# Kernel optimization log

Measured on AMD Instinct MI355X. Metric: run time of the kernel, lower is better.

The kernel has to match this reference:

```python
import jax, jax.numpy as jnp
import numpy as np

SEQ_LEN = 4096
N_FEAT = 2048
N_PADD = 128


def setup_inputs() -> dict:
    key = jax.random.key(0)
    kx, kw = jax.random.split(key)
    x = jax.random.normal(kx, (SEQ_LEN, N_FEAT), dtype=jnp.float32)
    # Fused QKV dense: features = 3 * n_feat
    W = jax.random.normal(kw, (N_FEAT, 3 * N_FEAT), dtype=jnp.float32) * (1.0 / np.sqrt(N_FEAT))
    b = jnp.zeros((3 * N_FEAT,), dtype=jnp.float32)
    return {"x": x, "W": W, "b": b, "n_padd": N_PADD}


def reference(x, W, b, n_padd):
    # Fused QKV projection, split along feature axis (as in nn.Dense + jnp.split)
    qkv = x @ W + b  # [S, 3F]
    q, k, v = jnp.split(qkv, 3, axis=1)  # each [S, F]
    S, F = q.shape
    idx = jnp.arange(S)
    # scores[i, j] = q_i . k_j / sqrt(F)
    scores = (q @ k.T) * (1.0 / jnp.sqrt(jnp.float32(F)))  # [S, S]
    seq_mask = idx >= n_padd                      # valid (non-padding) positions
    causal = idx[None, :] <= idx[:, None]         # j <= i
    mask = causal & seq_mask[None, :]             # kernel: causal_mask & seq_mask
    row_valid = seq_mask                          # rows < n_padd are not computed/stored
    neg_inf = jnp.float32(-jnp.inf)
    scores = jnp.where(mask, scores, neg_inf)
    # Fully-masked (padding) rows would softmax to NaN; neutralize then zero output.
    scores = jnp.where(row_valid[:, None], scores, 0.0)
    att = jax.nn.softmax(scores, axis=-1)         # row-wise stable softmax
    out = att @ v                                 # [S, F]
    out = jnp.where(row_valid[:, None], out, 0.0)  # padded rows produce zeros
    return out
```

## Files before the change

### kernel.cpp

```cpp
#include <hip/hip_runtime.h>
#include <cstdint>
#include <cstddef>
#include <cmath>

typedef unsigned short u16;
typedef short v8s __attribute__((ext_vector_type(8)));
typedef float v4f __attribute__((ext_vector_type(4)));

constexpr int SEQ = 4096;
constexpr int FEAT = 2048;
constexpr int F3 = 6144;


__device__ __forceinline__ u16 f2bf(float f) {
  union { float f; uint32_t u; } v; v.f = f;
  uint32_t r = v.u + 0x7FFFu + ((v.u >> 16) & 1u);
  return (u16)(r >> 16);
}

__device__ __forceinline__ float bf2f(u16 s) {
  union { uint32_t u; float f; } v; v.u = ((uint32_t)s) << 16;
  return v.f;
}

__device__ __forceinline__ void gld_lds16(const u16* g, u16* l) {
  __builtin_amdgcn_global_load_lds(
      (const __attribute__((address_space(1))) void*)g,
      (__attribute__((address_space(3))) void*)l, 16, 0, 0);
}


__global__ void cvt_f32_bf16(const float* __restrict__ in, u16* __restrict__ out, int n8) {
  int i = blockIdx.x * 256 + threadIdx.x;
  if (i >= n8) return;
  const float4* p = (const float4*)in + (size_t)i * 2;
  float4 a = p[0], b = p[1];
  union { u16 s[8]; uint4 v; } u;
  u.s[0] = f2bf(a.x); u.s[1] = f2bf(a.y); u.s[2] = f2bf(a.z); u.s[3] = f2bf(a.w);
  u.s[4] = f2bf(b.x); u.s[5] = f2bf(b.y); u.s[6] = f2bf(b.z); u.s[7] = f2bf(b.w);
  *(uint4*)(out + (size_t)i * 8) = u.v;
}

__global__ void transp_f2b(const float* __restrict__ in, int ldin,
                           u16* __restrict__ out, int ldout) {
  __shared__ float tile[32][33];
  int c0 = blockIdx.x * 32, r0 = blockIdx.y * 32;
  int tx = threadIdx.x, ty = threadIdx.y;
#pragma unroll
  for (int p = 0; p < 4; ++p)
    tile[ty + 8 * p][tx] = in[(size_t)(r0 + ty + 8 * p) * ldin + c0 + tx];
  __syncthreads();
#pragma unroll
  for (int p = 0; p < 4; ++p)
    out[(size_t)(c0 + ty + 8 * p) * ldout + r0 + tx] = f2bf(tile[tx][ty + 8 * p]);
}

__global__ void transp_b2b(const u16* __restrict__ in, int ldin,
                           u16* __restrict__ out, int ldout) {
  __shared__ u16 tile[32][33];
  int c0 = blockIdx.x * 32, r0 = blockIdx.y * 32;
  int tx = threadIdx.x, ty = threadIdx.y;
#pragma unroll
  for (int p = 0; p < 4; ++p)
    tile[ty + 8 * p][tx] = in[(size_t)(r0 + ty + 8 * p) * ldin + c0 + tx];
  __syncthreads();
#pragma unroll
  for (int p = 0; p < 4; ++p)
    out[(size_t)(c0 + ty + 8 * p) * ldout + r0 + tx] = tile[tx][ty + 8 * p];
}

__global__ __launch_bounds__(256) void add2_f32(
    const float* __restrict__ a, const float* __restrict__ b,
    float* __restrict__ o, int n4) {
  int i = blockIdx.x * 256 + threadIdx.x;
  if (i >= n4) return;
  float4 x = ((const float4*)a)[i], y = ((const float4*)b)[i];
  x.x += y.x; x.y += y.y; x.z += y.z; x.w += y.w;
  ((float4*)o)[i] = x;
}


#define BARW() asm volatile("s_barrier" ::: "memory")
#define VMC6() asm volatile("s_waitcnt vmcnt(6)" ::: "memory")
#define LGKM0() asm volatile("s_waitcnt lgkmcnt(0)" ::: "memory")

#define STAGE(SB, KO) do { \
  u16* Lb = &LDSU[SB][0] + w * 512; \
  gld_lds16(pA0 + (KO), Lb); \
  gld_lds16(pA0 + (size_t)64 * LDA_ + (KO), Lb + 2048); \
  gld_lds16(pB0 + (KO), Lb + 4096); \
  gld_lds16(pB0 + (size_t)64 * LDB_ + (KO), Lb + 4096 + 2048); \
  gld_lds16(pB0 + (size_t)128 * LDB_ + (KO), Lb + 4096 + 4096); \
  gld_lds16(pB0 + (size_t)192 * LDB_ + (KO), Lb + 4096 + 6144); \
} while (0)

#define LOADA(BUF) do { _Pragma("unroll") \
  for (int mi = 0; mi < 8; ++mi) \
    af[mi] = *(const v8s*)(&LDSU[BUF][0] + (mi * 16 + lm) * 32 + lqs); \
} while (0)

#define LOADB(BUF) do { _Pragma("unroll") \
  for (int ni = 0; ni < 4; ++ni) \
    bf4[ni] = *(const v8s*)(&LDSU[BUF][0] + 4096 + (w * 64 + ni * 16 + lm) * 32 + lqs); \
} while (0)

template<int LDA_, int LDB_, int LDC_, int OUTMODE ,
         int ADDB, int MODE, int SWZ>
__global__ __launch_bounds__(256, 2) void gemmw(
    const u16* __restrict__ A, const u16* __restrict__ B,
    void* __restrict__ Cv, int K,
    const float* __restrict__ bias, float scale) {
  int bi, bj, ks, ke;
  if (MODE == 1) {
    const int f = blockIdx.x;
    const int d3 = (f >> 3) & 1;
    const int par = (f & 1) ^ d3;
    const int p = (f >> 4) & 15;
    const int z = f >> 8;
    bi = par ? p : 31 - p;
    bj = ((f >> 1) & 3) | (d3 << 2);
    const int kq = (bi + 1) * 64;
    ks = z ? kq : 0;  ke = ks + kq;
    Cv = (void*)((float*)Cv + (size_t)z * SEQ * FEAT);
  } else {
    if (SWZ) {
      const int gx = gridDim.x, gy = gridDim.y;
      const int b = blockIdx.y * gx + blockIdx.x;
      const int cpx = (gx * gy) >> 3;
      const int s = (b & 7) * cpx + (b >> 3);
      bi = s % gy;  bj = s / gy;
    } else { bj = blockIdx.x; bi = blockIdx.y; }
    ks = 0; ke = K;
  }
  const int i0 = bi * 128, j0 = bj * 256;

  __shared__ u16 LDSU[3][12288];

  const int t = threadIdx.x;
  const int w = t >> 6, l = t & 63;
  const int lm = l & 15, lq = l >> 4;
  const int lqs = ((lq + (lm >> 1)) & 3) * 8;

  const int rA = w * 16 + (l >> 2);
  const int cA = ((((l & 3) - ((rA >> 1) & 3)) & 3)) * 8;
  const u16* pA0 = A + (size_t)(i0 + rA) * LDA_ + cA;
  const u16* pB0 = B + (size_t)(j0 + rA) * LDB_ + cA;

  v4f acc[8][4];
#pragma unroll
  for (int a = 0; a < 8; ++a)
#pragma unroll
    for (int b2 = 0; b2 < 4; ++b2)
      acc[a][b2] = v4f{0.f, 0.f, 0.f, 0.f};

  v8s af[8], bf4[4];

  STAGE(0, ks); STAGE(1, ks + 32);
  VMC6(); BARW();
  LOADB(0);

  const int nt = (ke - ks) >> 5;
  int b0 = 0, b1 = 1;
  for (int tt = 0; tt < nt; tt += 2) {
    const int kc = ks + (tt << 5);
    const int s2 = 3 - b0 - b1;
    {
      const int kst = (kc + 64 < ke) ? kc + 64 : ks;
      STAGE(s2, kst);
      LOADA(b0);
      __builtin_amdgcn_s_setprio(1);
#pragma unroll
      for (int mi = 0; mi < 8; ++mi)
#pragma unroll
        for (int ni = 0; ni < 4; ++ni)
          acc[mi][ni] = __builtin_amdgcn_mfma_f32_16x16x32_bf16(af[mi], bf4[ni], acc[mi][ni], 0, 0, 0);
      __builtin_amdgcn_s_setprio(0);
      VMC6(); BARW();
      LOADB(b1);
    }
    {
      const int kst = (kc + 96 < ke) ? kc + 96 : ks;
      STAGE(b0, kst);
      LOADA(b1);
      __builtin_amdgcn_s_setprio(1);
#pragma unroll
      for (int mi = 0; mi < 8; ++mi)
#pragma unroll
        for (int ni = 0; ni < 4; ++ni)
          acc[mi][ni] = __builtin_amdgcn_mfma_f32_16x16x32_bf16(af[mi], bf4[ni], acc[mi][ni], 0, 0, 0);
      __builtin_amdgcn_s_setprio(0);
      VMC6(); BARW();
      LOADB(s2);
    }
    b1 = b0; b0 = s2;
  }

#pragma unroll
  for (int mi = 0; mi < 8; ++mi) {
#pragma unroll
    for (int ni = 0; ni < 4; ++ni) {
      const int cc = j0 + w * 64 + ni * 16 + lm;
      const float badd = ADDB ? bias[cc] : 0.f;
#pragma unroll
      for (int r = 0; r < 4; ++r) {
        const int rr = i0 + mi * 16 + lq * 4 + r;
        if (OUTMODE == 0)
          ((u16*)Cv)[(size_t)rr * LDC_ + cc] = f2bf(acc[mi][ni][r] * scale + badd);
        else
          ((float*)Cv)[(size_t)rr * LDC_ + cc] = acc[mi][ni][r];
      }
    }
  }
}

#undef STAGE
#undef LOADA
#undef LOADB


#define LDA8(BUF, MH) do { _Pragma("unroll") \
  for (int fi = 0; fi < 4; ++fi) { \
    const u16* ap = &As8[BUF][wr][(MH) * 4096 + fi * 1024]; \
    af[fi][0] = *(const v8s*)(ap + off0); \
    af[fi][1] = *(const v8s*)(ap + off1); \
  } } while (0)

#define LDB8(BUF) do { _Pragma("unroll") \
  for (int ni = 0; ni < 4; ++ni) { \
    const u16* bp = &Bs8[BUF][bh][bo + ni * 1024]; \
    bfr[ni][0] = *(const v8s*)(bp + off0); \
    bfr[ni][1] = *(const v8s*)(bp + off1); \
  } } while (0)

#define MMA8(MH, NL) do { _Pragma("unroll") \
  for (int fi = 0; fi < 4; ++fi) { _Pragma("unroll") \
    for (int nn = 0; nn < 2; ++nn) { \
      acc[(MH)*4+fi][(NL)+nn] = __builtin_amdgcn_mfma_f32_16x16x32_bf16( \
          af[fi][0], bfr[(NL)+nn][0], acc[(MH)*4+fi][(NL)+nn], 0, 0, 0); \
      acc[(MH)*4+fi][(NL)+nn] = __builtin_amdgcn_mfma_f32_16x16x32_bf16( \
          af[fi][1], bfr[(NL)+nn][1], acc[(MH)*4+fi][(NL)+nn], 0, 0, 0); \
    } } } while (0)

#define STG8A(BUF, H, KO) do { \
  gld_lds16(Ag + (size_t)(H) * 128 * LDA_ + (KO), &As8[BUF][H][w8 * 1024]); \
  gld_lds16(Ag + ((size_t)(H) * 128 + 8) * LDA_ + (KO), &As8[BUF][H][w8 * 1024 + 512]); \
  } while (0)

#define STG8B(BUF, H, KO) do { \
  gld_lds16(Bg + (size_t)(H) * 128 * LDB_ + (KO), &Bs8[BUF][H][w8 * 1024]); \
  gld_lds16(Bg + ((size_t)(H) * 128 + 8) * LDB_ + (KO), &Bs8[BUF][H][w8 * 1024 + 512]); \
  } while (0)

template<int LDA_, int LDB_, int LDC_>
__global__ __launch_bounds__(512, 2) void gemm8tri(
    const u16* __restrict__ A, const u16* __restrict__ B,
    u16* __restrict__ C, int K, float scale) {
  const int b = blockIdx.x;
  const int cpx = (int)gridDim.x >> 3;
  const int s = (b & 7) * cpx + (b >> 3);
  int bi = (int)((sqrtf(8.f * s + 1.f) - 1.f) * 0.5f);
  while ((bi + 1) * (bi + 2) / 2 <= s) ++bi;
  while (bi * (bi + 1) / 2 > s) --bi;
  const int bj = s - bi * (bi + 1) / 2;
  const int i0 = bi * 256, j0 = bj * 256;

  __shared__ u16 As8[2][2][8192];
  __shared__ u16 Bs8[2][2][8192];

  const int t = threadIdx.x;
  const int w8 = t >> 6, l = t & 63;
  const int wr = w8 >> 2, wc = w8 & 3;
  const int lm = l & 15, lq = l >> 4;
  const int bh = wc >> 1, bo = (wc & 1) * 4096;

  const int off0 = lm * 64 + ((lq + lm) & 7) * 8;
  const int off1 = lm * 64 + ((lq + lm + 4) & 7) * 8;

  const int srow = w8 * 16 + (l >> 3);
  const int scol = (((l & 7) - (l >> 3)) & 7) * 8;
  const u16* Ag = A + (size_t)(i0 + srow) * LDA_ + scol;
  const u16* Bg = B + (size_t)(j0 + srow) * LDB_ + scol;

  v4f acc[8][4];
#pragma unroll
  for (int a = 0; a < 8; ++a)
#pragma unroll
    for (int b2 = 0; b2 < 4; ++b2)
      acc[a][b2] = v4f{0.f, 0.f, 0.f, 0.f};

  v8s af[4][2], bfr[4][2];

  STG8B(0, 0, 0); STG8B(0, 1, 0); STG8A(0, 0, 0); STG8A(0, 1, 0);
  STG8B(1, 0, 64); STG8B(1, 1, 64); STG8A(1, 0, 64);
  VMC6(); BARW();

  const int nit = K >> 7;
  for (int it = 0; it < nit; ++it) {
    const int kc = it << 7;
    const int k1 = kc + 64;
    int k2 = kc + 128; if (k2 >= K) k2 = 0;
    int k3 = kc + 192; if (k3 >= K) k3 = 0;

    LDA8(0, 0); LDB8(0);
    STG8A(1, 1, k1);
    BARW(); LGKM0();
    __builtin_amdgcn_s_setprio(1); MMA8(0, 0); __builtin_amdgcn_s_setprio(0);
    BARW();
    STG8B(0, 0, k2);
    BARW();
    __builtin_amdgcn_s_setprio(1); MMA8(0, 2); __builtin_amdgcn_s_setprio(0);
    BARW();
    LDA8(0, 1);
    STG8B(0, 1, k2);
    BARW(); LGKM0();
    __builtin_amdgcn_s_setprio(1); MMA8(1, 0); __builtin_amdgcn_s_setprio(0);
    BARW();
    STG8A(0, 0, k2);
    BARW();
    __builtin_amdgcn_s_setprio(1); MMA8(1, 2); __builtin_amdgcn_s_setprio(0);
    VMC6(); BARW();
    LDA8(1, 0); LDB8(1);
    STG8A(0, 1, k2);
    BARW(); LGKM0();
    __builtin_amdgcn_s_setprio(1); MMA8(0, 0); __builtin_amdgcn_s_setprio(0);
    BARW();
    STG8B(1, 0, k3);
    BARW();
    __builtin_amdgcn_s_setprio(1); MMA8(0, 2); __builtin_amdgcn_s_setprio(0);
    BARW();
    LDA8(1, 1);
    STG8B(1, 1, k3);
    BARW(); LGKM0();
    __builtin_amdgcn_s_setprio(1); MMA8(1, 0); __builtin_amdgcn_s_setprio(0);
    BARW();
    STG8A(1, 0, k3);
    BARW();
    __builtin_amdgcn_s_setprio(1); MMA8(1, 2); __builtin_amdgcn_s_setprio(0);
    VMC6(); BARW();
  }

#pragma unroll
  for (int mi = 0; mi < 8; ++mi) {
#pragma unroll
    for (int ni = 0; ni < 4; ++ni) {
      const int cc = j0 + wc * 64 + ni * 16 + lm;
#pragma unroll
      for (int r = 0; r < 4; ++r) {
        const int rr = i0 + wr * 128 + mi * 16 + lq * 4 + r;
        C[(size_t)rr * LDC_ + cc] = f2bf(acc[mi][ni][r] * scale);
      }
    }
  }
}

#undef LDA8
#undef LDB8
#undef MMA8
#undef STG8A
#undef STG8B

__global__ __launch_bounds__(256) void softmax_rows(
    const u16* __restrict__ S0,
    u16* __restrict__ att, const int* __restrict__ npad_p) {
  const int i = blockIdx.x;
  const int np = *npad_p;
  const int kend = ((i >> 7) + 1) << 7;
  const u16* r0 = S0 + (size_t)i * SEQ;
  u16* arow = att + (size_t)i * SEQ;
  const int t = threadIdx.x;

  float m = -3.0e38f, s = 0.f;
  for (int j0b = t * 8; j0b < kend; j0b += 2048) {
    union { u16 s8[8]; uint4 v; } ui;
    ui.v = *(const uint4*)(r0 + j0b);
#pragma unroll
    for (int q = 0; q < 8; ++q) {
      const int j = j0b + q;
      if (j >= np && j <= i) {
        const float v = bf2f(ui.s8[q]);
        if (v > m) { s = s * __expf(m - v) + 1.f; m = v; }
        else       { s += __expf(v - m); }
      }
    }
  }
#pragma unroll
  for (int off = 32; off > 0; off >>= 1) {
    float mo = __shfl_xor(m, off);
    float so = __shfl_xor(s, off);
    float M = fmaxf(m, mo);
    s = s * __expf(m - M) + so * __expf(mo - M);
    m = M;
  }
  __shared__ float sm[4], ss[4];
  const int w = t >> 6, l = t & 63;
  if (l == 0) { sm[w] = m; ss[w] = s; }
  __syncthreads();
  const float M = fmaxf(fmaxf(sm[0], sm[1]), fmaxf(sm[2], sm[3]));
  const float Ssum = ss[0] * __expf(sm[0] - M) + ss[1] * __expf(sm[1] - M) +
                     ss[2] * __expf(sm[2] - M) + ss[3] * __expf(sm[3] - M);
  const float inv = 1.f / Ssum;

  for (int j0b = t * 8; j0b < kend; j0b += 2048) {
    union { u16 s8[8]; uint4 v; } ui, uo;
    ui.v = *(const uint4*)(r0 + j0b);
#pragma unroll
    for (int q = 0; q < 8; ++q) {
      const int j = j0b + q;
      float a = 0.f;
      if (j >= np && j <= i)
        a = __expf(bf2f(ui.s8[q]) - M) * inv;
      uo.s8[q] = f2bf(a);
    }
    *(uint4*)(arow + j0b) = uo.v;
  }
}


extern "C" void kernel_launch(void* const* d_in, const int* in_sizes, int n_in,
                              void* d_out, int out_size, void* d_ws, size_t ws_size,
                              hipStream_t stream) {
  const float* x = (const float*)d_in[0];
  const float* W = (const float*)d_in[1];
  const float* b = (const float*)d_in[2];
  const int* npad = (const int*)d_in[3];
  float* out = (float*)d_out;

  char* p = (char*)d_ws;
  u16* xb = (u16*)p;
  u16* Wt = (u16*)(p + (size_t)SEQ * FEAT * 2);
  u16* att = (u16*)p;
  p += (size_t)SEQ * FEAT * 2 + (size_t)F3 * FEAT * 2;
  u16* qkvb = (u16*)p;  p += (size_t)SEQ * F3 * 2;
  u16* vt   = (u16*)p;  p += (size_t)FEAT * SEQ * 2;
  u16* sc0  = (u16*)p;  p += (size_t)SEQ * SEQ * 2;
  p += (size_t)SEQ * SEQ * 2;
  if (ws_size < (size_t)(p - (char*)d_ws)) return;

  float* p0 = (float*)sc0;
  float* p1 = p0 + (size_t)SEQ * FEAT;

  const float scale = 0.02209708691207961f;

  cvt_f32_bf16<<<SEQ * FEAT / 8 / 256, 256, 0, stream>>>(x, xb, SEQ * FEAT / 8);
  transp_f2b<<<dim3(F3 / 32, FEAT / 32), dim3(32, 8), 0, stream>>>(W, F3, Wt, FEAT);
  gemmw<FEAT, FEAT, F3, 0, 1, 0, 1><<<dim3(F3 / 256, SEQ / 128), 256, 0, stream>>>(
      xb, Wt, (void*)qkvb, FEAT, b, 1.0f);
  transp_b2b<<<dim3(FEAT / 32, SEQ / 32), dim3(32, 8), 0, stream>>>(
      qkvb + 2 * FEAT, F3, vt, SEQ);
  gemm8tri<F3, F3, SEQ><<<dim3(136), 512, 0, stream>>>(
      qkvb, qkvb + FEAT, sc0, FEAT, scale);
  softmax_rows<<<SEQ, 256, 0, stream>>>(sc0, att, npad);
  gemmw<SEQ, SEQ, FEAT, 1, 0, 1, 0><<<dim3(512), 256, 0, stream>>>(
      att, vt, (void*)p0, 0, nullptr, 1.0f);
  add2_f32<<<SEQ * FEAT / 4 / 256, 256, 0, stream>>>(p0, p1, out, SEQ * FEAT / 4);
}
```

Measured before the change: 391.8 us.

## Balance causal P@V work across 256 blocks and use two-pass softmax reduction

Measured after the change: 376.2 us. 1.04x faster.

```diff
diff --git a/kernel.cpp b/kernel.cpp
--- a/kernel.cpp
+++ b/kernel.cpp
@@ -74,9 +74,12 @@
     float* __restrict__ o, int n4) {
   int i = blockIdx.x * 256 + threadIdx.x;
   if (i >= n4) return;
-  float4 x = ((const float4*)a)[i], y = ((const float4*)b)[i];
-  x.x += y.x; x.y += y.y; x.z += y.z; x.w += y.w;
-  ((float4*)o)[i] = x;
+  float4 y = ((const float4*)b)[i];
+  if (i >= 2048 * (FEAT / 4)) {
+    float4 x = ((const float4*)a)[i];
+    y.x += x.x; y.y += x.y; y.z += x.z; y.w += x.w;
+  }
+  ((float4*)o)[i] = y;
 }
 
 
@@ -110,19 +113,28 @@
     const u16* __restrict__ A, const u16* __restrict__ B,
     void* __restrict__ Cv, int K,
     const float* __restrict__ bias, float scale) {
-  int bi, bj, ks, ke;
+  int bj;
+  int sI0[2], sKs[2], sKe[2];
+  float* sC[2] = {nullptr, nullptr};
+  int nseg;
   if (MODE == 1) {
     const int f = blockIdx.x;
-    const int d3 = (f >> 3) & 1;
-    const int par = (f & 1) ^ d3;
-    const int p = (f >> 4) & 15;
-    const int z = f >> 8;
-    bi = par ? p : 31 - p;
-    bj = ((f >> 1) & 3) | (d3 << 2);
-    const int kq = (bi + 1) * 64;
-    ks = z ? kq : 0;  ke = ks + kq;
-    Cv = (void*)((float*)Cv + (size_t)z * SEQ * FEAT);
+    const int p = f & 15;
+    bj = (f >> 4) & 7;
+    const int wi = f >> 7;
+    const int d = 31 - p;
+    float* p0 = (float*)Cv;
+    float* p1 = p0 + (size_t)SEQ * FEAT;
+    if (wi == 0) {
+      nseg = 1;
+      sI0[0] = d * 128; sKs[0] = 0;    sKe[0] = 2112;           sC[0] = p0;
+    } else {
+      nseg = 2;
+      sI0[0] = d * 128; sKs[0] = 2112; sKe[0] = (d + 1) * 128;  sC[0] = p1;
+      sI0[1] = p * 128; sKs[1] = 0;    sKe[1] = (p + 1) * 128;  sC[1] = p1;
+    }
   } else {
+    int bi;
     if (SWZ) {
       const int gx = gridDim.x, gy = gridDim.y;
       const int b = blockIdx.y * gx + blockIdx.x;
@@ -130,9 +142,10 @@
       const int s = (b & 7) * cpx + (b >> 3);
       bi = s % gy;  bj = s / gy;
     } else { bj = blockIdx.x; bi = blockIdx.y; }
-    ks = 0; ke = K;
-  }
-  const int i0 = bi * 128, j0 = bj * 256;
+    nseg = 1;
+    sI0[0] = bi * 128; sKs[0] = 0; sKe[0] = K; sC[0] = nullptr;
+  }
+  const int j0 = bj * 256;
 
   __shared__ u16 LDSU[3][12288];
 
@@ -143,74 +156,80 @@
 
   const int rA = w * 16 + (l >> 2);
   const int cA = ((((l & 3) - ((rA >> 1) & 3)) & 3)) * 8;
-  const u16* pA0 = A + (size_t)(i0 + rA) * LDA_ + cA;
   const u16* pB0 = B + (size_t)(j0 + rA) * LDB_ + cA;
 
-  v4f acc[8][4];
-#pragma unroll
-  for (int a = 0; a < 8; ++a)
-#pragma unroll
-    for (int b2 = 0; b2 < 4; ++b2)
-      acc[a][b2] = v4f{0.f, 0.f, 0.f, 0.f};
-
-  v8s af[8], bf4[4];
-
-  STAGE(0, ks); STAGE(1, ks + 32);
-  VMC6(); BARW();
-  LOADB(0);
-
-  const int nt = (ke - ks) >> 5;
-  int b0 = 0, b1 = 1;
-  for (int tt = 0; tt < nt; tt += 2) {
-    const int kc = ks + (tt << 5);
-    const int s2 = 3 - b0 - b1;
-    {
-      const int kst = (kc + 64 < ke) ? kc + 64 : ks;
-      STAGE(s2, kst);
-      LOADA(b0);
-      __builtin_amdgcn_s_setprio(1);
-#pragma unroll
-      for (int mi = 0; mi < 8; ++mi)
-#pragma unroll
-        for (int ni = 0; ni < 4; ++ni)
-          acc[mi][ni] = __builtin_amdgcn_mfma_f32_16x16x32_bf16(af[mi], bf4[ni], acc[mi][ni], 0, 0, 0);
-      __builtin_amdgcn_s_setprio(0);
-      VMC6(); BARW();
-      LOADB(b1);
-    }
-    {
-      const int kst = (kc + 96 < ke) ? kc + 96 : ks;
-      STAGE(b0, kst);
-      LOADA(b1);
-      __builtin_amdgcn_s_setprio(1);
-#pragma unroll
-      for (int mi = 0; mi < 8; ++mi)
-#pragma unroll
-        for (int ni = 0; ni < 4; ++ni)
-          acc[mi][ni] = __builtin_amdgcn_mfma_f32_16x16x32_bf16(af[mi], bf4[ni], acc[mi][ni], 0, 0, 0);
-      __builtin_amdgcn_s_setprio(0);
-      VMC6(); BARW();
-      LOADB(s2);
-    }
-    b1 = b0; b0 = s2;
-  }
-
-#pragma unroll
-  for (int mi = 0; mi < 8; ++mi) {
-#pragma unroll
-    for (int ni = 0; ni < 4; ++ni) {
-      const int cc = j0 + w * 64 + ni * 16 + lm;
-      const float badd = ADDB ? bias[cc] : 0.f;
-#pragma unroll
-      for (int r = 0; r < 4; ++r) {
-        const int rr = i0 + mi * 16 + lq * 4 + r;
-        if (OUTMODE == 0)
-          ((u16*)Cv)[(size_t)rr * LDC_ + cc] = f2bf(acc[mi][ni][r] * scale + badd);
-        else
-          ((float*)Cv)[(size_t)rr * LDC_ + cc] = acc[mi][ni][r];
+  auto run_seg = [&](int i0, int ks, int ke, float* Cf) {
+    const u16* pA0 = A + (size_t)(i0 + rA) * LDA_ + cA;
+
+    v4f acc[8][4];
+#pragma unroll
+    for (int a = 0; a < 8; ++a)
+#pragma unroll
+      for (int b2 = 0; b2 < 4; ++b2)
+        acc[a][b2] = v4f{0.f, 0.f, 0.f, 0.f};
+
+    v8s af[8], bf4[4];
+
+    STAGE(0, ks); STAGE(1, ks + 32);
+    VMC6(); BARW();
+    LOADB(0);
+
+    const int nt = (ke - ks) >> 5;
+    int b0 = 0, b1 = 1;
+    for (int tt = 0; tt < nt; tt += 2) {
+      const int kc = ks + (tt << 5);
+      const int s2 = 3 - b0 - b1;
+      {
+        const int kst = (kc + 64 < ke) ? kc + 64 : ks;
+        STAGE(s2, kst);
+        LOADA(b0);
+        __builtin_amdgcn_s_setprio(1);
+#pragma unroll
+        for (int mi = 0; mi < 8; ++mi)
+#pragma unroll
+          for (int ni = 0; ni < 4; ++ni)
+            acc[mi][ni] = __builtin_amdgcn_mfma_f32_16x16x32_bf16(af[mi], bf4[ni], acc[mi][ni], 0, 0, 0);
+        __builtin_amdgcn_s_setprio(0);
+        VMC6(); BARW();
+        LOADB(b1);
       }
-    }
-  }
+      {
+        const int kst = (kc + 96 < ke) ? kc + 96 : ks;
+        STAGE(b0, kst);
+        LOADA(b1);
+        __builtin_amdgcn_s_setprio(1);
+#pragma unroll
+        for (int mi = 0; mi < 8; ++mi)
+#pragma unroll
+          for (int ni = 0; ni < 4; ++ni)
+            acc[mi][ni] = __builtin_amdgcn_mfma_f32_16x16x32_bf16(af[mi], bf4[ni], acc[mi][ni], 0, 0, 0);
+        __builtin_amdgcn_s_setprio(0);
+        VMC6(); BARW();
+        LOADB(s2);
+      }
+      b1 = b0; b0 = s2;
+    }
+
+#pragma unroll
+    for (int mi = 0; mi < 8; ++mi) {
+#pragma unroll
+      for (int ni = 0; ni < 4; ++ni) {
+        const int cc = j0 + w * 64 + ni * 16 + lm;
+        const float badd = ADDB ? bias[cc] : 0.f;
+#pragma unroll
+        for (int r = 0; r < 4; ++r) {
+          const int rr = i0 + mi * 16 + lq * 4 + r;
+          if (OUTMODE == 0)
+            ((u16*)Cv)[(size_t)rr * LDC_ + cc] = f2bf(acc[mi][ni][r] * scale + badd);
+          else
+            Cf[(size_t)rr * LDC_ + cc] = acc[mi][ni][r];
+        }
+      }
+    }
+  };
+
+  run_seg(sI0[0], sKs[0], sKe[0], sC[0]);
+  if (nseg == 2) run_seg(sI0[1], sKs[1], sKe[1], sC[1]);
 }
 
 #undef STAGE
@@ -368,37 +387,42 @@
   const u16* r0 = S0 + (size_t)i * SEQ;
   u16* arow = att + (size_t)i * SEQ;
   const int t = threadIdx.x;
-
-  float m = -3.0e38f, s = 0.f;
+  const int w = t >> 6, l = t & 63;
+  __shared__ float sm[4], ss[4];
+
+  float m = -3.0e38f;
   for (int j0b = t * 8; j0b < kend; j0b += 2048) {
     union { u16 s8[8]; uint4 v; } ui;
     ui.v = *(const uint4*)(r0 + j0b);
 #pragma unroll
     for (int q = 0; q < 8; ++q) {
       const int j = j0b + q;
-      if (j >= np && j <= i) {
-        const float v = bf2f(ui.s8[q]);
-        if (v > m) { s = s * __expf(m - v) + 1.f; m = v; }
-        else       { s += __expf(v - m); }
-      }
-    }
-  }
-#pragma unroll
-  for (int off = 32; off > 0; off >>= 1) {
-    float mo = __shfl_xor(m, off);
-    float so = __shfl_xor(s, off);
-    float M = fmaxf(m, mo);
-    s = s * __expf(m - M) + so * __expf(mo - M);
-    m = M;
-  }
-  __shared__ float sm[4], ss[4];
-  const int w = t >> 6, l = t & 63;
-  if (l == 0) { sm[w] = m; ss[w] = s; }
+      const float v = (j >= np && j <= i) ? bf2f(ui.s8[q]) : -3.0e38f;
+      m = fmaxf(m, v);
+    }
+  }
+#pragma unroll
+  for (int off = 32; off > 0; off >>= 1) m = fmaxf(m, __shfl_xor(m, off));
+  if (l == 0) sm[w] = m;
   __syncthreads();
   const float M = fmaxf(fmaxf(sm[0], sm[1]), fmaxf(sm[2], sm[3]));
-  const float Ssum = ss[0] * __expf(sm[0] - M) + ss[1] * __expf(sm[1] - M) +
-                     ss[2] * __expf(sm[2] - M) + ss[3] * __expf(sm[3] - M);
-  const float inv = 1.f / Ssum;
+
+  float s = 0.f;
+  for (int j0b = t * 8; j0b < kend; j0b += 2048) {
+    union { u16 s8[8]; uint4 v; } ui;
+    ui.v = *(const uint4*)(r0 + j0b);
+#pragma unroll
+    for (int q = 0; q < 8; ++q) {
+      const int j = j0b + q;
+      const float v = (j >= np && j <= i) ? bf2f(ui.s8[q]) : -3.0e38f;
+      s += __expf(v - M);
+    }
+  }
+#pragma unroll
+  for (int off = 32; off > 0; off >>= 1) s += __shfl_xor(s, off);
+  if (l == 0) ss[w] = s;
+  __syncthreads();
+  const float inv = 1.f / (ss[0] + ss[1] + ss[2] + ss[3]);
 
   for (int j0b = t * 8; j0b < kend; j0b += 2048) {
     union { u16 s8[8]; uint4 v; } ui, uo;
@@ -450,7 +474,7 @@
   gemm8tri<F3, F3, SEQ><<<dim3(136), 512, 0, stream>>>(
       qkvb, qkvb + FEAT, sc0, FEAT, scale);
   softmax_rows<<<SEQ, 256, 0, stream>>>(sc0, att, npad);
-  gemmw<SEQ, SEQ, FEAT, 1, 0, 1, 0><<<dim3(512), 256, 0, stream>>>(
+  gemmw<SEQ, SEQ, FEAT, 1, 0, 1, 0><<<dim3(256), 256, 0, stream>>>(
       att, vt, (void*)p0, 0, nullptr, 1.0f);
   add2_f32<<<SEQ * FEAT / 4 / 256, 256, 0, stream>>>(p0, p1, out, SEQ * FEAT / 4);
 }
```
